# Performance work log

Measured on AMD Instinct MI355X. Metric: run time of the kernel, lower is better.

The kernel has to match this reference:

```python
import jax, jax.numpy as jnp
import numpy as np

B, H, W, D = 64, 32, 32, 64
K = 1024  # codebook_size


def setup_inputs() -> dict:
    key = jax.random.key(0)
    kz, ke = jax.random.split(key)
    z = jax.random.normal(kz, (B, H, W, D), dtype=jnp.float32)
    embeddings = 0.02 * jax.random.normal(ke, (K, D), dtype=jnp.float32)
    return {"z": z, "embeddings": embeddings}


def reference(z, embeddings):
    # Flatten spatial/batch dims: (N, D) with N = B*H*W
    z_flat = z.reshape(-1, z.shape[-1])
    # Squared euclidean distances via ||a||^2 + ||b||^2 - 2 a.b  -> (N, K)
    distances = (jnp.sum(z_flat ** 2, axis=1, keepdims=True)
                 + jnp.sum(embeddings ** 2, axis=1)
                 - 2.0 * jnp.dot(z_flat, embeddings.T))
    indices = jnp.argmin(distances, axis=1)  # (N,)
    quantized = embeddings[indices].reshape(z.shape)  # (B, H, W, D)
    indices = indices.reshape(z.shape[0], z.shape[1], z.shape[2])  # (B, H, W)
    return quantized, indices
```

## Files before the change

kernel.cpp:

```cpp
#include <hip/hip_runtime.h>

#define NPTS   65536
#define DDIM   64
#define KCODES 1024
#define QOUT_ELEMS (NPTS * DDIM)

typedef _Float16 half8    __attribute__((ext_vector_type(8)));
typedef float    floatx16 __attribute__((ext_vector_type(16)));
typedef unsigned int uint;

#define AS1 __attribute__((address_space(1)))
#define AS3 __attribute__((address_space(3)))

#define WS_EHP   0
#define WS_ELP   (128*1024)
#define WS_E2    (256*1024)

union H8U { half8 v; uint u[4]; };

static __device__ __forceinline__ void gl_lds16(const void* g, void* l) {
    __builtin_amdgcn_global_load_lds((const AS1 uint*)g, (AS3 uint*)l, 16, 0, 0);
}

__global__ void eprep_kernel(const float* __restrict__ emb, char* __restrict__ ws) {
    const int tid = threadIdx.x;
    const int w = tid >> 6, d = tid & 63;
    const int k = blockIdx.x * 4 + w;
    float v = emb[(size_t)k * DDIM + d];
    _Float16 h = (_Float16)v;
    _Float16 l = (_Float16)(v - (float)h);
    size_t off = (size_t)(k >> 5) * 4096 + (size_t)(d >> 3) * 512
               + (size_t)(k & 31) * 16 + (size_t)(d & 7) * 2;
    *(_Float16*)(ws + WS_EHP + off) = h;
    *(_Float16*)(ws + WS_ELP + off) = l;
    float s = v * v;
    #pragma unroll
    for (int m = 1; m < 64; m <<= 1) s += __shfl_xor(s, m, 64);
    if (d == 0) {
        _Float16 e2h = (_Float16)s;
        _Float16 e2l = (_Float16)(s - (float)e2h);
        unsigned short hb = *(unsigned short*)&e2h;
        unsigned short lb = *(unsigned short*)&e2l;
        ((uint*)(ws + WS_E2))[k] = (uint)hb | ((uint)lb << 16);
    }
}

__global__ __launch_bounds__(256, 3) void vq_kernel(
    const float* __restrict__ z,
    const char* __restrict__ ws_c,
    const float* __restrict__ emb,
    float* __restrict__ out)
{
    const int tid  = threadIdx.x;
    const int lane = tid & 63;
    const int w    = __builtin_amdgcn_readfirstlane(tid >> 6);
    const int col  = lane & 31;
    const int sel8 = lane >> 5;
    const int pgrp = blockIdx.x;

    __shared__ uint4 ldseh[256];
    __shared__ uint4 ldsel[256];
    __shared__ uint  lds_e2[1024];
    __shared__ int   s_final[128];

    const int pt = pgrp * 128 + w * 32 + col;
    half8 ah[4], al[4];
    {
        const float* zrow = z + (size_t)pt * DDIM + sel8 * 8;
        #pragma unroll
        for (int ks = 0; ks < 4; ++ks) {
            float4 u0 = *(const float4*)(zrow + ks * 16);
            float4 u1 = *(const float4*)(zrow + ks * 16 + 4);
            float tv[8] = {u0.x, u0.y, u0.z, u0.w, u1.x, u1.y, u1.z, u1.w};
            #pragma unroll
            for (int j = 0; j < 8; ++j) {
                float a = -2.0f * tv[j];
                _Float16 hh = (_Float16)a;
                ah[ks][j] = hh;
                al[ks][j] = (_Float16)(a - (float)hh);
            }
        }
    }
    half8 ahE;
    { H8U t0; t0.u[0] = (sel8 == 0) ? 0x3C003C00u : 0u;
      t0.u[1] = t0.u[2] = t0.u[3] = 0u; ahE = t0.v; }

    gl_lds16(ws_c + WS_E2 + w * 1024 + lane * 16, (char*)lds_e2 + w * 1024);

    const floatx16 zeroC = {};

    float best[16];
    int   bt[16];
    #pragma unroll
    for (int r = 0; r < 16; ++r) { best[r] = 3.4e38f; bt[r] = 0; }

    const int myoff = sel8 * 512 + col * 16;

    for (int t = 0; t < 32; ++t) {
        __syncthreads();
        {
            const int opnd = w >> 1, half = w & 1;
            const char* src = ws_c + (opnd ? WS_ELP : WS_EHP)
                            + (size_t)t * 4096 + half * 2048 + lane * 16;
            char* dst = (char*)(opnd ? ldsel : ldseh) + half * 2048;
            gl_lds16(src, dst);
            gl_lds16(src + 1024, dst + 1024);
        }
        __syncthreads();

        const char* ehb = (const char*)ldseh + myoff;
        const char* elb = (const char*)ldsel + myoff;
        half8 bh[4], bl[4];
        #pragma unroll
        for (int ks = 0; ks < 4; ++ks) {
            bh[ks] = *(const half8*)(ehb + ks * 1024);
            bl[ks] = *(const half8*)(elb + ks * 1024);
        }
        half8 bhE;
        { H8U u; u.u[0] = lds_e2[t * 32 + col];
          u.u[1] = u.u[2] = u.u[3] = 0u; bhE = u.v; }

        floatx16 acc = __builtin_amdgcn_mfma_f32_32x32x16_f16(ah[0], bh[0], zeroC, 0, 0, 0);
        acc = __builtin_amdgcn_mfma_f32_32x32x16_f16(ah[1], bh[1], acc, 0, 0, 0);
        acc = __builtin_amdgcn_mfma_f32_32x32x16_f16(ah[2], bh[2], acc, 0, 0, 0);
        acc = __builtin_amdgcn_mfma_f32_32x32x16_f16(ah[3], bh[3], acc, 0, 0, 0);
        acc = __builtin_amdgcn_mfma_f32_32x32x16_f16(ahE,  bhE,  acc, 0, 0, 0);
        acc = __builtin_amdgcn_mfma_f32_32x32x16_f16(ah[0], bl[0], acc, 0, 0, 0);
        acc = __builtin_amdgcn_mfma_f32_32x32x16_f16(ah[1], bl[1], acc, 0, 0, 0);
        acc = __builtin_amdgcn_mfma_f32_32x32x16_f16(ah[2], bl[2], acc, 0, 0, 0);
        acc = __builtin_amdgcn_mfma_f32_32x32x16_f16(ah[3], bl[3], acc, 0, 0, 0);
        acc = __builtin_amdgcn_mfma_f32_32x32x16_f16(al[0], bh[0], acc, 0, 0, 0);
        acc = __builtin_amdgcn_mfma_f32_32x32x16_f16(al[1], bh[1], acc, 0, 0, 0);
        acc = __builtin_amdgcn_mfma_f32_32x32x16_f16(al[2], bh[2], acc, 0, 0, 0);
        acc = __builtin_amdgcn_mfma_f32_32x32x16_f16(al[3], bh[3], acc, 0, 0, 0);

        #pragma unroll
        for (int r = 0; r < 16; ++r) {
            bool c = acc[r] < best[r];
            best[r] = c ? acc[r] : best[r];
            bt[r]   = c ? t      : bt[r];
        }
    }

    int code[16];
    #pragma unroll
    for (int r = 0; r < 16; ++r) code[r] = bt[r] * 32 + col;
    #pragma unroll
    for (int m = 1; m < 32; m <<= 1) {
        #pragma unroll
        for (int r = 0; r < 16; ++r) {
            float ov = __shfl_xor(best[r], m, 64);
            int   oc = __shfl_xor(code[r], m, 64);
            bool c = (ov < best[r]) || (ov == best[r] && oc < code[r]);
            best[r] = c ? ov : best[r];
            code[r] = c ? oc : code[r];
        }
    }
    if (col == 0) {
        #pragma unroll
        for (int r = 0; r < 16; ++r) {
            int row = (r & 3) + 8 * (r >> 2) + 4 * sel8;
            s_final[w * 32 + row] = code[r];
        }
    }
    __syncthreads();

    if (tid < 128)
        out[QOUT_ELEMS + (size_t)pgrp * 128 + tid] = (float)s_final[tid];
    float4* outq = (float4*)out;
    const float4* emb4 = (const float4*)emb;
    #pragma unroll
    for (int it = 0; it < 8; ++it) {
        int f  = it * 256 + tid;
        int p  = f >> 4;
        int d4 = f & 15;
        int ks = s_final[p];
        outq[((size_t)pgrp * 128 + p) * (DDIM / 4) + d4] =
            emb4[(size_t)ks * (DDIM / 4) + d4];
    }
}

extern "C" void kernel_launch(void* const* d_in, const int* in_sizes, int n_in,
                              void* d_out, int out_size, void* d_ws, size_t ws_size,
                              hipStream_t stream) {
    const float* z   = (const float*)d_in[0];
    const float* emb = (const float*)d_in[1];
    float* out = (float*)d_out;
    char* ws = (char*)d_ws;

    eprep_kernel<<<KCODES / 4, 256, 0, stream>>>(emb, ws);
    vq_kernel<<<NPTS / 128, 256, 0, stream>>>(z, ws, emb, out);
}
```

Measured before the change: 104.0 us.

## Load codebook tiles directly to registers with double-buffered prefetch

Drops the LDS staging of codebook tiles and the two barriers per tile. Each wave now loads its B operands and the e2 terms straight from global memory (L2-resident) into registers, double-buffered so the next tile's loads overlap the current tile's MFMAs. It also splits the MFMA chain into two independent accumulators to shorten the dependency chain, raises MFMA priority with s_setprio, and lowers launch bounds from 3 to 2 waves per SIMD because of the extra registers. The risks are redundant global/L2 traffic, since every wave reloads the full codebook, and lower occupancy. The split-accumulator sum also changes rounding order slightly.

```diff
diff --git a/kernel.cpp b/kernel.cpp
--- a/kernel.cpp
+++ b/kernel.cpp
@@ -9,18 +9,11 @@
 typedef float    floatx16 __attribute__((ext_vector_type(16)));
 typedef unsigned int uint;
 
-#define AS1 __attribute__((address_space(1)))
-#define AS3 __attribute__((address_space(3)))
-
 #define WS_EHP   0
 #define WS_ELP   (128*1024)
 #define WS_E2    (256*1024)
 
 union H8U { half8 v; uint u[4]; };
-
-static __device__ __forceinline__ void gl_lds16(const void* g, void* l) {
-    __builtin_amdgcn_global_load_lds((const AS1 uint*)g, (AS3 uint*)l, 16, 0, 0);
-}
 
 __global__ void eprep_kernel(const float* __restrict__ emb, char* __restrict__ ws) {
     const int tid = threadIdx.x;
@@ -45,7 +38,9 @@
     }
 }
 
-__global__ __launch_bounds__(256, 3) void vq_kernel(
+#define MFMA(A,B,C) __builtin_amdgcn_mfma_f32_32x32x16_f16(A,B,C,0,0,0)
+
+__global__ __launch_bounds__(256, 2) void vq_kernel(
     const float* __restrict__ z,
     const char* __restrict__ ws_c,
     const float* __restrict__ emb,
@@ -58,10 +53,7 @@
     const int sel8 = lane >> 5;
     const int pgrp = blockIdx.x;
 
-    __shared__ uint4 ldseh[256];
-    __shared__ uint4 ldsel[256];
-    __shared__ uint  lds_e2[1024];
-    __shared__ int   s_final[128];
+    __shared__ int s_final[128];
 
     const int pt = pgrp * 128 + w * 32 + col;
     half8 ah[4], al[4];
@@ -85,8 +77,6 @@
     { H8U t0; t0.u[0] = (sel8 == 0) ? 0x3C003C00u : 0u;
       t0.u[1] = t0.u[2] = t0.u[3] = 0u; ahE = t0.v; }
 
-    gl_lds16(ws_c + WS_E2 + w * 1024 + lane * 16, (char*)lds_e2 + w * 1024);
-
     const floatx16 zeroC = {};
 
     float best[16];
@@ -95,52 +85,59 @@
     for (int r = 0; r < 16; ++r) { best[r] = 3.4e38f; bt[r] = 0; }
 
     const int myoff = sel8 * 512 + col * 16;
+    const char* ebase = ws_c + myoff;
+    const uint* e2p   = (const uint*)(ws_c + WS_E2);
 
-    for (int t = 0; t < 32; ++t) {
-        __syncthreads();
-        {
-            const int opnd = w >> 1, half = w & 1;
-            const char* src = ws_c + (opnd ? WS_ELP : WS_EHP)
-                            + (size_t)t * 4096 + half * 2048 + lane * 16;
-            char* dst = (char*)(opnd ? ldsel : ldseh) + half * 2048;
-            gl_lds16(src, dst);
-            gl_lds16(src + 1024, dst + 1024);
-        }
-        __syncthreads();
+    half8 bhA[4], blA[4], bhB[4], blB[4];
+    uint  eA, eB;
 
-        const char* ehb = (const char*)ldseh + myoff;
-        const char* elb = (const char*)ldsel + myoff;
-        half8 bh[4], bl[4];
-        #pragma unroll
-        for (int ks = 0; ks < 4; ++ks) {
-            bh[ks] = *(const half8*)(ehb + ks * 1024);
-            bl[ks] = *(const half8*)(elb + ks * 1024);
-        }
-        half8 bhE;
-        { H8U u; u.u[0] = lds_e2[t * 32 + col];
-          u.u[1] = u.u[2] = u.u[3] = 0u; bhE = u.v; }
+#define LOADT(T, BH, BL, E2) do {                                        \
+    const char* _b = ebase + (size_t)(T) * 4096;                         \
+    _Pragma("unroll")                                                    \
+    for (int ks = 0; ks < 4; ++ks) {                                     \
+        BH[ks] = *(const half8*)(_b + ks * 1024);                        \
+        BL[ks] = *(const half8*)(_b + WS_ELP + ks * 1024);               \
+    }                                                                    \
+    E2 = e2p[(T) * 32 + col];                                            \
+} while (0)
 
-        floatx16 acc = __builtin_amdgcn_mfma_f32_32x32x16_f16(ah[0], bh[0], zeroC, 0, 0, 0);
-        acc = __builtin_amdgcn_mfma_f32_32x32x16_f16(ah[1], bh[1], acc, 0, 0, 0);
-        acc = __builtin_amdgcn_mfma_f32_32x32x16_f16(ah[2], bh[2], acc, 0, 0, 0);
-        acc = __builtin_amdgcn_mfma_f32_32x32x16_f16(ah[3], bh[3], acc, 0, 0, 0);
-        acc = __builtin_amdgcn_mfma_f32_32x32x16_f16(ahE,  bhE,  acc, 0, 0, 0);
-        acc = __builtin_amdgcn_mfma_f32_32x32x16_f16(ah[0], bl[0], acc, 0, 0, 0);
-        acc = __builtin_amdgcn_mfma_f32_32x32x16_f16(ah[1], bl[1], acc, 0, 0, 0);
-        acc = __builtin_amdgcn_mfma_f32_32x32x16_f16(ah[2], bl[2], acc, 0, 0, 0);
-        acc = __builtin_amdgcn_mfma_f32_32x32x16_f16(ah[3], bl[3], acc, 0, 0, 0);
-        acc = __builtin_amdgcn_mfma_f32_32x32x16_f16(al[0], bh[0], acc, 0, 0, 0);
-        acc = __builtin_amdgcn_mfma_f32_32x32x16_f16(al[1], bh[1], acc, 0, 0, 0);
-        acc = __builtin_amdgcn_mfma_f32_32x32x16_f16(al[2], bh[2], acc, 0, 0, 0);
-        acc = __builtin_amdgcn_mfma_f32_32x32x16_f16(al[3], bh[3], acc, 0, 0, 0);
+#define TILE(T, BH, BL, E2) do {                                         \
+    H8U _u; _u.u[0] = (E2); _u.u[1] = _u.u[2] = _u.u[3] = 0u;            \
+    __builtin_amdgcn_s_setprio(1);                                       \
+    floatx16 _a0 = MFMA(ah[0], BH[0], zeroC);                            \
+    _a0 = MFMA(ah[1], BH[1], _a0);                                       \
+    _a0 = MFMA(ah[2], BH[2], _a0);                                       \
+    _a0 = MFMA(ah[3], BH[3], _a0);                                       \
+    _a0 = MFMA(ahE,   _u.v,  _a0);                                       \
+    floatx16 _a1 = MFMA(ah[0], BL[0], zeroC);                            \
+    _a1 = MFMA(ah[1], BL[1], _a1);                                       \
+    _a1 = MFMA(ah[2], BL[2], _a1);                                       \
+    _a1 = MFMA(ah[3], BL[3], _a1);                                       \
+    _a1 = MFMA(al[0], BH[0], _a1);                                       \
+    _a1 = MFMA(al[1], BH[1], _a1);                                       \
+    _a1 = MFMA(al[2], BH[2], _a1);                                       \
+    _a1 = MFMA(al[3], BH[3], _a1);                                       \
+    __builtin_amdgcn_s_setprio(0);                                       \
+    _Pragma("unroll")                                                    \
+    for (int r = 0; r < 16; ++r) {                                       \
+        float _d = _a0[r] + _a1[r];                                      \
+        bool  _c = _d < best[r];       \
+        best[r] = _c ? _d  : best[r];                                    \
+        bt[r]   = _c ? (T) : bt[r];                                      \
+    }                                                                    \
+} while (0)
 
-        #pragma unroll
-        for (int r = 0; r < 16; ++r) {
-            bool c = acc[r] < best[r];
-            best[r] = c ? acc[r] : best[r];
-            bt[r]   = c ? t      : bt[r];
-        }
+    LOADT(0, bhA, blA, eA);
+    for (int t = 0; t < 32; t += 2) {
+        LOADT(t + 1, bhB, blB, eB);
+        TILE(t, bhA, blA, eA);
+        int tn = (t + 2 < 32) ? (t + 2) : 0;
+        LOADT(tn, bhA, blA, eA);
+        TILE(t + 1, bhB, blB, eB);
     }
+
+#undef LOADT
+#undef TILE
 
     int code[16];
     #pragma unroll
```

Result: slower. 108.1 us (+4.0%).

## Split codebook across wave pairs with double-buffered LDS staging and merge

Applied to the files above, without the earlier changes.

Each block now handles 64 points instead of 128. The two wave pairs each scan half of the codebook (16 tiles), and the partial argmins are merged through shared memory. Embedding tiles are double-buffered in LDS, so the global-to-LDS load of the next tile overlaps the MFMA work on the current one, and the loop needs one barrier per iteration instead of two. MFMA sections run at raised wave priority, the grid size doubles, and the occupancy hint rises to 4. In exchange, every block rereads half the codebook for half as many points, so codebook traffic per point doubles, and ties across the two halves are broken by comparing distances (preferring the lower half on equality).

```diff
diff --git a/kernel.cpp b/kernel.cpp
--- a/kernel.cpp
+++ b/kernel.cpp
@@ -45,25 +45,31 @@
     }
 }
 
-__global__ __launch_bounds__(256, 3) void vq_kernel(
+#define MFMA(A,B,C) __builtin_amdgcn_mfma_f32_32x32x16_f16(A,B,C,0,0,0)
+
+__global__ __launch_bounds__(256, 4) void vq_kernel(
     const float* __restrict__ z,
     const char* __restrict__ ws_c,
     const float* __restrict__ emb,
     float* __restrict__ out)
 {
-    const int tid  = threadIdx.x;
-    const int lane = tid & 63;
-    const int w    = __builtin_amdgcn_readfirstlane(tid >> 6);
-    const int col  = lane & 31;
-    const int sel8 = lane >> 5;
-    const int pgrp = blockIdx.x;
-
-    __shared__ uint4 ldseh[256];
-    __shared__ uint4 ldsel[256];
+    const int tid   = threadIdx.x;
+    const int lane  = tid & 63;
+    const int w     = __builtin_amdgcn_readfirstlane(tid >> 6);
+    const int col   = lane & 31;
+    const int sel8  = lane >> 5;
+    const int pgrp  = blockIdx.x;
+    const int pair  = w >> 1;
+    const int phalf = w & 1;
+    const int tbase = pair * 16;
+
+    __shared__ char  ebuf[2][2][8192];
     __shared__ uint  lds_e2[1024];
-    __shared__ int   s_final[128];
-
-    const int pt = pgrp * 128 + w * 32 + col;
+    __shared__ float sbest[2][64];
+    __shared__ int   scode[2][64];
+    __shared__ int   s_final[64];
+
+    const int pt = pgrp * 64 + phalf * 32 + col;
     half8 ah[4], al[4];
     {
         const float* zrow = z + (size_t)pt * DDIM + sel8 * 8;
@@ -85,8 +91,6 @@
     { H8U t0; t0.u[0] = (sel8 == 0) ? 0x3C003C00u : 0u;
       t0.u[1] = t0.u[2] = t0.u[3] = 0u; ahE = t0.v; }
 
-    gl_lds16(ws_c + WS_E2 + w * 1024 + lane * 16, (char*)lds_e2 + w * 1024);
-
     const floatx16 zeroC = {};
 
     float best[16];
@@ -94,45 +98,53 @@
     #pragma unroll
     for (int r = 0; r < 16; ++r) { best[r] = 3.4e38f; bt[r] = 0; }
 
+    gl_lds16(ws_c + WS_E2 + w * 1024 + lane * 16, (char*)lds_e2 + w * 1024);
+
+#define STAGE(CUR, T) do {                                                    \
+    const char* _s = ws_c + (phalf ? WS_ELP : WS_EHP)                         \
+                   + (size_t)(tbase + (T)) * 4096 + lane * 16;                \
+    char* _d = &ebuf[pair][CUR][phalf * 4096] + lane * 16;                    \
+    gl_lds16(_s,        _d);                                                  \
+    gl_lds16(_s + 1024, _d + 1024);                                           \
+    gl_lds16(_s + 2048, _d + 2048);                                           \
+    gl_lds16(_s + 3072, _d + 3072);                                           \
+} while (0)
+
+    STAGE(0, 0);
+    __syncthreads();
+
     const int myoff = sel8 * 512 + col * 16;
 
-    for (int t = 0; t < 32; ++t) {
-        __syncthreads();
-        {
-            const int opnd = w >> 1, half = w & 1;
-            const char* src = ws_c + (opnd ? WS_ELP : WS_EHP)
-                            + (size_t)t * 4096 + half * 2048 + lane * 16;
-            char* dst = (char*)(opnd ? ldsel : ldseh) + half * 2048;
-            gl_lds16(src, dst);
-            gl_lds16(src + 1024, dst + 1024);
-        }
-        __syncthreads();
-
-        const char* ehb = (const char*)ldseh + myoff;
-        const char* elb = (const char*)ldsel + myoff;
+    for (int t = 0; t < 16; ++t) {
+        const int cur = t & 1;
+        if (t < 15) STAGE(cur ^ 1, t + 1);
+
+        const char* bb = &ebuf[pair][cur][0] + myoff;
         half8 bh[4], bl[4];
         #pragma unroll
         for (int ks = 0; ks < 4; ++ks) {
-            bh[ks] = *(const half8*)(ehb + ks * 1024);
-            bl[ks] = *(const half8*)(elb + ks * 1024);
+            bh[ks] = *(const half8*)(bb + ks * 1024);
+            bl[ks] = *(const half8*)(bb + 4096 + ks * 1024);
         }
         half8 bhE;
-        { H8U u; u.u[0] = lds_e2[t * 32 + col];
+        { H8U u; u.u[0] = lds_e2[(tbase + t) * 32 + col];
           u.u[1] = u.u[2] = u.u[3] = 0u; bhE = u.v; }
 
-        floatx16 acc = __builtin_amdgcn_mfma_f32_32x32x16_f16(ah[0], bh[0], zeroC, 0, 0, 0);
-        acc = __builtin_amdgcn_mfma_f32_32x32x16_f16(ah[1], bh[1], acc, 0, 0, 0);
-        acc = __builtin_amdgcn_mfma_f32_32x32x16_f16(ah[2], bh[2], acc, 0, 0, 0);
-        acc = __builtin_amdgcn_mfma_f32_32x32x16_f16(ah[3], bh[3], acc, 0, 0, 0);
-        acc = __builtin_amdgcn_mfma_f32_32x32x16_f16(ahE,  bhE,  acc, 0, 0, 0);
-        acc = __builtin_amdgcn_mfma_f32_32x32x16_f16(ah[0], bl[0], acc, 0, 0, 0);
-        acc = __builtin_amdgcn_mfma_f32_32x32x16_f16(ah[1], bl[1], acc, 0, 0, 0);
-        acc = __builtin_amdgcn_mfma_f32_32x32x16_f16(ah[2], bl[2], acc, 0, 0, 0);
-        acc = __builtin_amdgcn_mfma_f32_32x32x16_f16(ah[3], bl[3], acc, 0, 0, 0);
-        acc = __builtin_amdgcn_mfma_f32_32x32x16_f16(al[0], bh[0], acc, 0, 0, 0);
-        acc = __builtin_amdgcn_mfma_f32_32x32x16_f16(al[1], bh[1], acc, 0, 0, 0);
-        acc = __builtin_amdgcn_mfma_f32_32x32x16_f16(al[2], bh[2], acc, 0, 0, 0);
-        acc = __builtin_amdgcn_mfma_f32_32x32x16_f16(al[3], bh[3], acc, 0, 0, 0);
+        __builtin_amdgcn_s_setprio(1);
+        floatx16 acc = MFMA(ah[0], bh[0], zeroC);
+        acc = MFMA(ah[1], bh[1], acc);
+        acc = MFMA(ah[2], bh[2], acc);
+        acc = MFMA(ah[3], bh[3], acc);
+        acc = MFMA(ahE,   bhE,  acc);
+        acc = MFMA(ah[0], bl[0], acc);
+        acc = MFMA(ah[1], bl[1], acc);
+        acc = MFMA(ah[2], bl[2], acc);
+        acc = MFMA(ah[3], bl[3], acc);
+        acc = MFMA(al[0], bh[0], acc);
+        acc = MFMA(al[1], bh[1], acc);
+        acc = MFMA(al[2], bh[2], acc);
+        acc = MFMA(al[3], bh[3], acc);
+        __builtin_amdgcn_s_setprio(0);
 
         #pragma unroll
         for (int r = 0; r < 16; ++r) {
@@ -140,11 +152,14 @@
             best[r] = c ? acc[r] : best[r];
             bt[r]   = c ? t      : bt[r];
         }
-    }
+
+        if (t < 15) __syncthreads();
+    }
+#undef STAGE
 
     int code[16];
     #pragma unroll
-    for (int r = 0; r < 16; ++r) code[r] = bt[r] * 32 + col;
+    for (int r = 0; r < 16; ++r) code[r] = (tbase + bt[r]) * 32 + col;
     #pragma unroll
     for (int m = 1; m < 32; m <<= 1) {
         #pragma unroll
@@ -156,26 +171,34 @@
             code[r] = c ? oc : code[r];
         }
     }
+    __syncthreads();
     if (col == 0) {
         #pragma unroll
         for (int r = 0; r < 16; ++r) {
             int row = (r & 3) + 8 * (r >> 2) + 4 * sel8;
-            s_final[w * 32 + row] = code[r];
-        }
-    }
-    __syncthreads();
-
-    if (tid < 128)
-        out[QOUT_ELEMS + (size_t)pgrp * 128 + tid] = (float)s_final[tid];
+            sbest[pair][phalf * 32 + row] = best[r];
+            scode[pair][phalf * 32 + row] = code[r];
+        }
+    }
+    __syncthreads();
+
+    if (tid < 64) {
+        float d0 = sbest[0][tid], d1 = sbest[1][tid];
+        s_final[tid] = (d1 < d0) ? scode[1][tid] : scode[0][tid];
+    }
+    __syncthreads();
+
+    if (tid < 64)
+        out[QOUT_ELEMS + (size_t)pgrp * 64 + tid] = (float)s_final[tid];
     float4* outq = (float4*)out;
     const float4* emb4 = (const float4*)emb;
     #pragma unroll
-    for (int it = 0; it < 8; ++it) {
+    for (int it = 0; it < 4; ++it) {
         int f  = it * 256 + tid;
         int p  = f >> 4;
         int d4 = f & 15;
         int ks = s_final[p];
-        outq[((size_t)pgrp * 128 + p) * (DDIM / 4) + d4] =
+        outq[((size_t)pgrp * 64 + p) * (DDIM / 4) + d4] =
             emb4[(size_t)ks * (DDIM / 4) + d4];
     }
 }
@@ -189,5 +212,5 @@
     char* ws = (char*)d_ws;
 
     eprep_kernel<<<KCODES / 4, 256, 0, stream>>>(emb, ws);
-    vq_kernel<<<NPTS / 128, 256, 0, stream>>>(z, ws, emb, out);
-}
+    vq_kernel<<<NPTS / 64, 256, 0, stream>>>(z, ws, emb, out);
+}
```

After: 110.2 us. +6.0%, slower.

## Double-buffer codebook tiles in LDS and split MFMA chain into two accumulators

Applied to the files above, without the earlier changes.

Replaces the single LDS staging buffer with a two-slot ping-pong buffer, so the global-to-LDS load of the next codebook tile overlaps the MFMA work on the current one, and halves the barriers per tile. The serial 13-MFMA dependency chain becomes two independent accumulator chains of six, and the ||e||^2 term is added in fp32 after the MFMAs instead of through an extra MFMA, so the eprep kernel now stores it as a plain float. It also raises MFMA priority around the compute block and lowers the occupancy hint from 3 to 2 blocks per SM. The cost is higher register pressure and fewer resident blocks.

```diff
diff --git a/kernel.cpp b/kernel.cpp
--- a/kernel.cpp
+++ b/kernel.cpp
@@ -15,8 +15,6 @@
 #define WS_EHP   0
 #define WS_ELP   (128*1024)
 #define WS_E2    (256*1024)
-
-union H8U { half8 v; uint u[4]; };
 
 static __device__ __forceinline__ void gl_lds16(const void* g, void* l) {
     __builtin_amdgcn_global_load_lds((const AS1 uint*)g, (AS3 uint*)l, 16, 0, 0);
@@ -36,16 +34,12 @@
     float s = v * v;
     #pragma unroll
     for (int m = 1; m < 64; m <<= 1) s += __shfl_xor(s, m, 64);
-    if (d == 0) {
-        _Float16 e2h = (_Float16)s;
-        _Float16 e2l = (_Float16)(s - (float)e2h);
-        unsigned short hb = *(unsigned short*)&e2h;
-        unsigned short lb = *(unsigned short*)&e2l;
-        ((uint*)(ws + WS_E2))[k] = (uint)hb | ((uint)lb << 16);
-    }
-}
-
-__global__ __launch_bounds__(256, 3) void vq_kernel(
+    if (d == 0) ((float*)(ws + WS_E2))[k] = s;
+}
+
+#define MFMA(A,B,C) __builtin_amdgcn_mfma_f32_32x32x16_f16(A,B,C,0,0,0)
+
+__global__ __launch_bounds__(256, 2) void vq_kernel(
     const float* __restrict__ z,
     const char* __restrict__ ws_c,
     const float* __restrict__ emb,
@@ -58,9 +52,8 @@
     const int sel8 = lane >> 5;
     const int pgrp = blockIdx.x;
 
-    __shared__ uint4 ldseh[256];
-    __shared__ uint4 ldsel[256];
-    __shared__ uint  lds_e2[1024];
+    __shared__ char  ebuf[2][8192];
+    __shared__ float lds_e2[1024];
     __shared__ int   s_final[128];
 
     const int pt = pgrp * 128 + w * 32 + col;
@@ -81,11 +74,6 @@
             }
         }
     }
-    half8 ahE;
-    { H8U t0; t0.u[0] = (sel8 == 0) ? 0x3C003C00u : 0u;
-      t0.u[1] = t0.u[2] = t0.u[3] = 0u; ahE = t0.v; }
-
-    gl_lds16(ws_c + WS_E2 + w * 1024 + lane * 16, (char*)lds_e2 + w * 1024);
 
     const floatx16 zeroC = {};
 
@@ -94,53 +82,75 @@
     #pragma unroll
     for (int r = 0; r < 16; ++r) { best[r] = 3.4e38f; bt[r] = 0; }
 
+    gl_lds16(ws_c + WS_E2 + w * 1024 + lane * 16, (char*)lds_e2 + w * 1024);
+
+    const int opnd = w >> 1, hsel = w & 1;
+    const char* gsrc = ws_c + (opnd ? WS_ELP : WS_EHP) + hsel * 2048 + lane * 16;
+    char* ld0 = &ebuf[0][0] + opnd * 4096 + hsel * 2048 + lane * 16;
+    char* ld1 = &ebuf[1][0] + opnd * 4096 + hsel * 2048 + lane * 16;
+
+#define STAGE(BUF, T) do {                                                    \
+    const char* _s = gsrc + (size_t)(T) * 4096;                               \
+    char* _d = (BUF) ? ld1 : ld0;                                             \
+    gl_lds16(_s,        _d);                                                  \
+    gl_lds16(_s + 1024, _d + 1024);                                           \
+} while (0)
+
     const int myoff = sel8 * 512 + col * 16;
-
-    for (int t = 0; t < 32; ++t) {
+    const char* fb0 = &ebuf[0][0] + myoff;
+    const char* fb1 = &ebuf[1][0] + myoff;
+
+#define READF(BUF, T, BH, BL, E2) do {                                        \
+    const char* _b = (BUF) ? fb1 : fb0;                                       \
+    _Pragma("unroll")                                                         \
+    for (int ks = 0; ks < 4; ++ks) {                                          \
+        BH[ks] = *(const half8*)(_b + ks * 1024);                             \
+        BL[ks] = *(const half8*)(_b + 4096 + ks * 1024);                      \
+    }                                                                         \
+    E2 = lds_e2[(T) * 32 + col];                                              \
+} while (0)
+
+#define COMP(T, BH, BL, E2) do {                                              \
+    __builtin_amdgcn_s_setprio(1);                                            \
+    floatx16 c0 = MFMA(ah[0], BH[0], zeroC);                                  \
+    floatx16 c1 = MFMA(ah[0], BL[0], zeroC);                                  \
+    c0 = MFMA(ah[1], BH[1], c0);  c1 = MFMA(ah[1], BL[1], c1);                \
+    c0 = MFMA(ah[2], BH[2], c0);  c1 = MFMA(ah[2], BL[2], c1);                \
+    c0 = MFMA(ah[3], BH[3], c0);  c1 = MFMA(ah[3], BL[3], c1);                \
+    c0 = MFMA(al[0], BH[0], c0);  c1 = MFMA(al[2], BH[2], c1);                \
+    c0 = MFMA(al[1], BH[1], c0);  c1 = MFMA(al[3], BH[3], c1);                \
+    __builtin_amdgcn_s_setprio(0);                                            \
+    _Pragma("unroll")                                                         \
+    for (int r = 0; r < 16; ++r) {                                            \
+        float d = (c0[r] + c1[r]) + (E2);                                     \
+        bool c = d < best[r];               \
+        best[r] = c ? d   : best[r];                                          \
+        bt[r]   = c ? (T) : bt[r];                                            \
+    }                                                                         \
+} while (0)
+
+    half8 bhA[4], blA[4], bhB[4], blB[4];
+    float e2A, e2B;
+
+    STAGE(0, 0);
+    __syncthreads();
+    READF(0, 0, bhA, blA, e2A);
+    STAGE(1, 1);
+
+    for (int t = 0; t < 32; t += 2) {
         __syncthreads();
-        {
-            const int opnd = w >> 1, half = w & 1;
-            const char* src = ws_c + (opnd ? WS_ELP : WS_EHP)
-                            + (size_t)t * 4096 + half * 2048 + lane * 16;
-            char* dst = (char*)(opnd ? ldsel : ldseh) + half * 2048;
-            gl_lds16(src, dst);
-            gl_lds16(src + 1024, dst + 1024);
-        }
+        READF(1, t + 1, bhB, blB, e2B);
+        if (t + 2 < 32) STAGE(0, t + 2);
+        COMP(t, bhA, blA, e2A);
+
         __syncthreads();
-
-        const char* ehb = (const char*)ldseh + myoff;
-        const char* elb = (const char*)ldsel + myoff;
-        half8 bh[4], bl[4];
-        #pragma unroll
-        for (int ks = 0; ks < 4; ++ks) {
-            bh[ks] = *(const half8*)(ehb + ks * 1024);
-            bl[ks] = *(const half8*)(elb + ks * 1024);
-        }
-        half8 bhE;
-        { H8U u; u.u[0] = lds_e2[t * 32 + col];
-          u.u[1] = u.u[2] = u.u[3] = 0u; bhE = u.v; }
-
-        floatx16 acc = __builtin_amdgcn_mfma_f32_32x32x16_f16(ah[0], bh[0], zeroC, 0, 0, 0);
-        acc = __builtin_amdgcn_mfma_f32_32x32x16_f16(ah[1], bh[1], acc, 0, 0, 0);
-        acc = __builtin_amdgcn_mfma_f32_32x32x16_f16(ah[2], bh[2], acc, 0, 0, 0);
-        acc = __builtin_amdgcn_mfma_f32_32x32x16_f16(ah[3], bh[3], acc, 0, 0, 0);
-        acc = __builtin_amdgcn_mfma_f32_32x32x16_f16(ahE,  bhE,  acc, 0, 0, 0);
-        acc = __builtin_amdgcn_mfma_f32_32x32x16_f16(ah[0], bl[0], acc, 0, 0, 0);
-        acc = __builtin_amdgcn_mfma_f32_32x32x16_f16(ah[1], bl[1], acc, 0, 0, 0);
-        acc = __builtin_amdgcn_mfma_f32_32x32x16_f16(ah[2], bl[2], acc, 0, 0, 0);
-        acc = __builtin_amdgcn_mfma_f32_32x32x16_f16(ah[3], bl[3], acc, 0, 0, 0);
-        acc = __builtin_amdgcn_mfma_f32_32x32x16_f16(al[0], bh[0], acc, 0, 0, 0);
-        acc = __builtin_amdgcn_mfma_f32_32x32x16_f16(al[1], bh[1], acc, 0, 0, 0);
-        acc = __builtin_amdgcn_mfma_f32_32x32x16_f16(al[2], bh[2], acc, 0, 0, 0);
-        acc = __builtin_amdgcn_mfma_f32_32x32x16_f16(al[3], bh[3], acc, 0, 0, 0);
-
-        #pragma unroll
-        for (int r = 0; r < 16; ++r) {
-            bool c = acc[r] < best[r];
-            best[r] = c ? acc[r] : best[r];
-            bt[r]   = c ? t      : bt[r];
-        }
-    }
+        if (t + 2 < 32) READF(0, t + 2, bhA, blA, e2A);
+        if (t + 3 < 32) STAGE(1, t + 3);
+        COMP(t + 1, bhB, blB, e2B);
+    }
+#undef STAGE
+#undef READF
+#undef COMP
 
     int code[16];
     #pragma unroll
```

New measurement: 103.2 us. No clear change (-0.8%).
